# Kernel tuning notes

Hardware: AMD Instinct MI355X
Metric: run time of the kernel (lower is better)

## Reference

```python
import jax, jax.numpy as jnp
import numpy as np

N_NODES = 100000


def _add_self_loops(edge_index, n):
    loops = jnp.arange(n, dtype=edge_index.dtype)
    src = jnp.concatenate([edge_index[0], loops])
    dst = jnp.concatenate([edge_index[1], loops])
    return src, dst


def _gcn_norm(src, dst, n):
    # symmetric normalization with unit edge weights (edge_weight=None)
    w = jnp.ones(src.shape[0], dtype=jnp.float32)
    deg = jax.ops.segment_sum(w, dst, num_segments=n)  # in-degree at dst (col)
    dinv = jnp.where(deg > 0, jax.lax.rsqrt(jnp.maximum(deg, 1.0)), 0.0)
    return dinv[src] * w * dinv[dst]


def _gcn_conv(x, W, b, src, dst, norm, n):
    h = x @ W                              # [N, F_out] linear first (as in PyG GCNConv)
    msg = h[src] * norm[:, None]           # gather + per-edge scale
    agg = jax.ops.segment_sum(msg, dst, num_segments=n)  # scatter-add at dst
    return agg + b


def setup_inputs() -> dict:
    key = jax.random.key(0)
    k1, k2, k3, k4 = jax.random.split(key, 4)
    x = jax.random.normal(k1, (N_NODES, 128), dtype=jnp.float32)
    edge_index = jax.random.randint(k2, (2, 1600000), 0, N_NODES, dtype=jnp.int64)
    W1 = jax.random.normal(k3, (128, 64), dtype=jnp.float32) * 0.08
    b1 = jnp.zeros((64,), dtype=jnp.float32)
    W2 = jax.random.normal(k4, (64, 40), dtype=jnp.float32) * 0.1
    b2 = jnp.zeros((40,), dtype=jnp.float32)
    return {"x": x, "edge_index": edge_index, "W1": W1, "b1": b1, "W2": W2, "b2": b2}


def reference(x, edge_index, W1, b1, W2, b2):
    n = x.shape[0]
    src, dst = _add_self_loops(edge_index, n)
    norm = _gcn_norm(src, dst, n)
    h = _gcn_conv(x, W1, b1, src, dst, norm, n)
    h = jax.nn.relu(h)
    # dropout is identity in eval mode (training=False)
    out = _gcn_conv(h, W2, b2, src, dst, norm, n)
    return out
```

## Files before the change

kernel.cpp:

```cpp
#include <hip/hip_runtime.h>
#include <hip/hip_fp16.h>


#define NPB   128
#define NBCAP 1024


__global__ void k_zero(int* __restrict__ p, int m) {
    int i = blockIdx.x * blockDim.x + threadIdx.x;
    if (i < m) p[i] = 0;
}

__global__ __launch_bounds__(256) void k_hist(const int* __restrict__ dst, int E,
                                              int* __restrict__ bcnt, int nb) {
    __shared__ int h[NBCAP];
    for (int i = threadIdx.x; i < nb; i += 256) h[i] = 0;
    __syncthreads();
    int stride = gridDim.x * 256;
    for (int e = blockIdx.x * 256 + threadIdx.x; e < E; e += stride)
        atomicAdd(&h[dst[e] >> 7], 1);
    __syncthreads();
    for (int i = threadIdx.x; i < nb; i += 256)
        if (h[i]) atomicAdd(&bcnt[i], h[i]);
}

__global__ __launch_bounds__(1024) void k_scan_nb(const int* __restrict__ bcnt,
                                                  int* __restrict__ bbase,
                                                  int* __restrict__ bcur, int nb) {
    __shared__ int tmp[NBCAP];
    int t = threadIdx.x;
    int v = (t < nb) ? bcnt[t] : 0;
    tmp[t] = v;
    __syncthreads();
    for (int ofs = 1; ofs < NBCAP; ofs <<= 1) {
        int u = (t >= ofs) ? tmp[t - ofs] : 0;
        __syncthreads();
        if (t >= ofs) tmp[t] += u;
        __syncthreads();
    }
    if (t < nb) {
        int ex = tmp[t] - v;
        bbase[t] = ex;
        bcur[t] = ex;
        if (t == nb - 1) bbase[nb] = tmp[t];
    }
}

__global__ __launch_bounds__(256) void k_binpass(const int* __restrict__ src,
                                                 const int* __restrict__ dst,
                                                 int* __restrict__ bcur,
                                                 int* __restrict__ pairs,
                                                 int nb, int E) {
    __shared__ int lh[NBCAP];
    __shared__ int lbase[NBCAP];
    for (int i = threadIdx.x; i < nb; i += 256) lh[i] = 0;
    __syncthreads();
    int base = blockIdx.x * 4096;
    int pk[16], bb[16];
#pragma unroll
    for (int k = 0; k < 16; ++k) {
        int e = base + k * 256 + threadIdx.x;
        if (e < E) {
            int d = dst[e];
            int b = d >> 7;
            bb[k] = b;
            pk[k] = src[e] | ((d & (NPB - 1)) << 17);
            atomicAdd(&lh[b], 1);
        } else bb[k] = -1;
    }
    __syncthreads();
    for (int i = threadIdx.x; i < nb; i += 256) {
        int c = lh[i];
        lbase[i] = c ? atomicAdd(&bcur[i], c) : 0;
        lh[i] = 0;
    }
    __syncthreads();
#pragma unroll
    for (int k = 0; k < 16; ++k) {
        if (bb[k] >= 0) {
            int r = atomicAdd(&lh[bb[k]], 1);
            pairs[lbase[bb[k]] + r] = pk[k];
        }
    }
}

__global__ __launch_bounds__(256) void k_bucket_build(const int* __restrict__ pairs,
                                                      const int* __restrict__ bbase,
                                                      int* __restrict__ off,
                                                      int* __restrict__ csrc,
                                                      float* __restrict__ dinv,
                                                      int n, int nb) {
    __shared__ int deg[NPB], sc[NPB], cur[NPB];
    int t = threadIdx.x;
    int bid = blockIdx.x;
    int node0 = bid * NPB;
    int ebeg = bbase[bid], eend = bbase[bid + 1];
    if (t < NPB) deg[t] = 0;
    __syncthreads();
    for (int e = ebeg + t; e < eend; e += 256)
        atomicAdd(&deg[pairs[e] >> 17], 1);
    __syncthreads();
    if (t < NPB) sc[t] = deg[t];
    __syncthreads();
    for (int ofs = 1; ofs < NPB; ofs <<= 1) {
        int u = (t < NPB && t >= ofs) ? sc[t - ofs] : 0;
        __syncthreads();
        if (t < NPB && t >= ofs) sc[t] += u;
        __syncthreads();
    }
    if (t < NPB) {
        int ex = sc[t] - deg[t];
        cur[t] = ex;
        int node = node0 + t;
        if (node < n) {
            off[node] = ebeg + ex;
            dinv[node] = rsqrtf((float)(deg[t] + 1));
        }
    }
    if (t == 0 && bid == nb - 1) off[n] = eend;
    __syncthreads();
    for (int e = ebeg + t; e < eend; e += 256) {
        int pkv = pairs[e];
        int r = atomicAdd(&cur[pkv >> 17], 1);
        csrc[ebeg + r] = pkv & 0x1FFFF;
    }
}


union pk2 { __half2 h[2]; uint2 u; };

__device__ __forceinline__ void h4_acc(const __half* p, float4& a) {
    uint2 u = *(const uint2*)p;
    __half2 h0 = *(__half2*)&u.x, h1 = *(__half2*)&u.y;
    float2 f0 = __half22float2(h0), f1 = __half22float2(h1);
    a.x += f0.x; a.y += f0.y; a.z += f1.x; a.w += f1.y;
}

#define F4ADD(a, b) { (a).x += (b).x; (a).y += (b).y; (a).z += (b).z; (a).w += (b).w; }


__global__ __launch_bounds__(256) void k_gemm1_h(const float* __restrict__ x,
                                                 const float* __restrict__ W,
                                                 __half* __restrict__ h, int n,
                                                 const float* __restrict__ dinv) {
    __shared__ float Ws[128 * 64];
    __shared__ float xsT[128 * 64];
    const int tid = threadIdx.x;
    const int row0 = blockIdx.x * 64;
    {
        const float4* Wg = (const float4*)W;
        float4* Wl = (float4*)Ws;
#pragma unroll
        for (int t = 0; t < 8; ++t) Wl[tid + t * 256] = Wg[tid + t * 256];
    }
    {
        int r = tid & 63, g = tid >> 6;
        int row = row0 + r;
        const float4* xr = (const float4*)(x + (size_t)row * 128);
#pragma unroll
        for (int t = 0; t < 8; ++t) {
            int k0 = g * 32 + t * 4;
            float4 v = (row < n) ? xr[k0 >> 2] : make_float4(0.f, 0.f, 0.f, 0.f);
            xsT[(k0 + 0) * 64 + r] = v.x;
            xsT[(k0 + 1) * 64 + r] = v.y;
            xsT[(k0 + 2) * 64 + r] = v.z;
            xsT[(k0 + 3) * 64 + r] = v.w;
        }
    }
    __syncthreads();

    const int tc = tid & 15;
    const int rg = tid >> 4;
    float acc[4][4];
#pragma unroll
    for (int i = 0; i < 4; ++i)
#pragma unroll
        for (int j = 0; j < 4; ++j) acc[i][j] = 0.f;

#pragma unroll 4
    for (int k = 0; k < 128; ++k) {
        float4 a = *(const float4*)&xsT[k * 64 + rg * 4];
        float4 b = *(const float4*)&Ws[k * 64 + tc * 4];
        acc[0][0] += a.x * b.x; acc[0][1] += a.x * b.y; acc[0][2] += a.x * b.z; acc[0][3] += a.x * b.w;
        acc[1][0] += a.y * b.x; acc[1][1] += a.y * b.y; acc[1][2] += a.y * b.z; acc[1][3] += a.y * b.w;
        acc[2][0] += a.z * b.x; acc[2][1] += a.z * b.y; acc[2][2] += a.z * b.z; acc[2][3] += a.z * b.w;
        acc[3][0] += a.w * b.x; acc[3][1] += a.w * b.y; acc[3][2] += a.w * b.z; acc[3][3] += a.w * b.w;
    }

#pragma unroll
    for (int i = 0; i < 4; ++i) {
        int row = row0 + rg * 4 + i;
        if (row < n) {
            float dd = dinv[row];
            pk2 p;
            p.h[0] = __floats2half2_rn(acc[i][0] * dd, acc[i][1] * dd);
            p.h[1] = __floats2half2_rn(acc[i][2] * dd, acc[i][3] * dd);
            *(uint2*)&h[(size_t)row * 64 + tc * 4] = p.u;
        }
    }
}

__global__ __launch_bounds__(256) void k_gemm2_h(const __half* __restrict__ agg,
                                                 const float* __restrict__ W2,
                                                 __half* __restrict__ h2, int n,
                                                 const float* __restrict__ dinv) {
    __shared__ float Ws[64 * 40];
    __shared__ float hsT[64 * 64];
    const int tid = threadIdx.x;
    const int row0 = blockIdx.x * 64;
    {
        const float4* Wg = (const float4*)W2;
        float4* Wl = (float4*)Ws;
        for (int i = tid; i < 640; i += 256) Wl[i] = Wg[i];
    }
    {
        int r = tid & 63, g = tid >> 6;
        int row = row0 + r;
        const __half* ar = agg + (size_t)row * 64;
#pragma unroll
        for (int t = 0; t < 4; ++t) {
            int k0 = g * 16 + t * 4;
            float4 v = make_float4(0.f, 0.f, 0.f, 0.f);
            if (row < n) {
                uint2 u = *(const uint2*)(ar + k0);
                __half2 h0 = *(__half2*)&u.x, h1 = *(__half2*)&u.y;
                float2 f0 = __half22float2(h0), f1 = __half22float2(h1);
                v = make_float4(f0.x, f0.y, f1.x, f1.y);
            }
            hsT[(k0 + 0) * 64 + r] = v.x > 0.f ? v.x : 0.f;
            hsT[(k0 + 1) * 64 + r] = v.y > 0.f ? v.y : 0.f;
            hsT[(k0 + 2) * 64 + r] = v.z > 0.f ? v.z : 0.f;
            hsT[(k0 + 3) * 64 + r] = v.w > 0.f ? v.w : 0.f;
        }
    }
    __syncthreads();

    const int tc = tid & 15;
    const int rg = tid >> 4;
    if (tc < 10) {
        float acc[4][4];
#pragma unroll
        for (int i = 0; i < 4; ++i)
#pragma unroll
            for (int j = 0; j < 4; ++j) acc[i][j] = 0.f;

#pragma unroll 4
        for (int k = 0; k < 64; ++k) {
            float4 a = *(const float4*)&hsT[k * 64 + rg * 4];
            float4 b = *(const float4*)&Ws[k * 40 + tc * 4];
            acc[0][0] += a.x * b.x; acc[0][1] += a.x * b.y; acc[0][2] += a.x * b.z; acc[0][3] += a.x * b.w;
            acc[1][0] += a.y * b.x; acc[1][1] += a.y * b.y; acc[1][2] += a.y * b.z; acc[1][3] += a.y * b.w;
            acc[2][0] += a.z * b.x; acc[2][1] += a.z * b.y; acc[2][2] += a.z * b.z; acc[2][3] += a.z * b.w;
            acc[3][0] += a.w * b.x; acc[3][1] += a.w * b.y; acc[3][2] += a.w * b.z; acc[3][3] += a.w * b.w;
        }

#pragma unroll
        for (int i = 0; i < 4; ++i) {
            int row = row0 + rg * 4 + i;
            if (row < n) {
                float dd = dinv[row];
                pk2 p;
                p.h[0] = __floats2half2_rn(acc[i][0] * dd, acc[i][1] * dd);
                p.h[1] = __floats2half2_rn(acc[i][2] * dd, acc[i][3] * dd);
                *(uint2*)&h2[(size_t)row * 40 + tc * 4] = p.u;
            }
        }
    }
}


__global__ __launch_bounds__(256) void k_gather1_h(const __half* __restrict__ hs,
                                                   const int* __restrict__ off,
                                                   const int* __restrict__ csrc,
                                                   const float* __restrict__ dinv,
                                                   const float4* __restrict__ b1_4,
                                                   __half* __restrict__ agg, int n) {
    int node = blockIdx.x * 4 + (threadIdx.x >> 6);
    if (node >= n) return;
    int lane = threadIdx.x & 63;
    int g = lane >> 4, q = lane & 15;
    int beg = off[node], end = off[node + 1];
    float4 a0 = make_float4(0.f, 0.f, 0.f, 0.f);
    float4 a1 = make_float4(0.f, 0.f, 0.f, 0.f);
    float4 a2 = make_float4(0.f, 0.f, 0.f, 0.f);
    float4 a3 = make_float4(0.f, 0.f, 0.f, 0.f);
    int j = beg;
    for (; j + 16 <= end; j += 16) {
        int s0 = csrc[j + g], s1 = csrc[j + 4 + g];
        int s2 = csrc[j + 8 + g], s3 = csrc[j + 12 + g];
        h4_acc(hs + (size_t)s0 * 64 + q * 4, a0);
        h4_acc(hs + (size_t)s1 * 64 + q * 4, a1);
        h4_acc(hs + (size_t)s2 * 64 + q * 4, a2);
        h4_acc(hs + (size_t)s3 * 64 + q * 4, a3);
    }
    for (; j + 8 <= end; j += 8) {
        int s0 = csrc[j + g], s1 = csrc[j + 4 + g];
        h4_acc(hs + (size_t)s0 * 64 + q * 4, a0);
        h4_acc(hs + (size_t)s1 * 64 + q * 4, a1);
    }
    for (; j < end; j += 4) {
        int jj = j + g;
        if (jj < end) {
            int s = csrc[jj];
            h4_acc(hs + (size_t)s * 64 + q * 4, a0);
        }
    }
    F4ADD(a0, a1); F4ADD(a2, a3); F4ADD(a0, a2);
    a0.x += __shfl_down(a0.x, 32); a0.y += __shfl_down(a0.y, 32);
    a0.z += __shfl_down(a0.z, 32); a0.w += __shfl_down(a0.w, 32);
    a0.x += __shfl_down(a0.x, 16); a0.y += __shfl_down(a0.y, 16);
    a0.z += __shfl_down(a0.z, 16); a0.w += __shfl_down(a0.w, 16);
    if (lane < 16) {
        float4 s = make_float4(0.f, 0.f, 0.f, 0.f);
        h4_acc(hs + (size_t)node * 64 + q * 4, s);
        float dd = dinv[node];
        float4 b = b1_4[q];
        pk2 p;
        p.h[0] = __floats2half2_rn((a0.x + s.x) * dd + b.x, (a0.y + s.y) * dd + b.y);
        p.h[1] = __floats2half2_rn((a0.z + s.z) * dd + b.z, (a0.w + s.w) * dd + b.w);
        *(uint2*)&agg[(size_t)node * 64 + q * 4] = p.u;
    }
}

__global__ __launch_bounds__(256) void k_gather2_h(const __half* __restrict__ h2s,
                                                   const int* __restrict__ off,
                                                   const int* __restrict__ csrc,
                                                   const float* __restrict__ dinv,
                                                   const float4* __restrict__ b2_4,
                                                   float4* __restrict__ out4, int n) {
    int node = blockIdx.x * 4 + (threadIdx.x >> 6);
    if (node >= n) return;
    int lane = threadIdx.x & 63;
    int g = lane / 10;
    int q = lane - g * 10;
    bool act = g < 6;
    int beg = off[node], end = off[node + 1];
    float4 a0 = make_float4(0.f, 0.f, 0.f, 0.f);
    float4 a1 = make_float4(0.f, 0.f, 0.f, 0.f);
    int j = beg;
    for (; j + 12 <= end; j += 12) {
        if (act) {
            int s0 = csrc[j + g], s1 = csrc[j + 6 + g];
            h4_acc(h2s + (size_t)s0 * 40 + q * 4, a0);
            h4_acc(h2s + (size_t)s1 * 40 + q * 4, a1);
        }
    }
    for (; j < end; j += 6) {
        int jj = j + g;
        if (act && jj < end) {
            int s = csrc[jj];
            h4_acc(h2s + (size_t)s * 40 + q * 4, a0);
        }
    }
    F4ADD(a0, a1);
    float4 r;
    r.x = __shfl_down(a0.x, 30); r.y = __shfl_down(a0.y, 30);
    r.z = __shfl_down(a0.z, 30); r.w = __shfl_down(a0.w, 30);
    if (lane < 30) F4ADD(a0, r);
    r.x = __shfl_down(a0.x, 20); r.y = __shfl_down(a0.y, 20);
    r.z = __shfl_down(a0.z, 20); r.w = __shfl_down(a0.w, 20);
    if (lane < 10) F4ADD(a0, r);
    r.x = __shfl_down(a0.x, 10); r.y = __shfl_down(a0.y, 10);
    r.z = __shfl_down(a0.z, 10); r.w = __shfl_down(a0.w, 10);
    if (lane < 10) F4ADD(a0, r);
    if (lane < 10) {
        float4 s = make_float4(0.f, 0.f, 0.f, 0.f);
        h4_acc(h2s + (size_t)node * 40 + q * 4, s);
        float dd = dinv[node];
        float4 b = b2_4[q];
        float4 o;
        o.x = (a0.x + s.x) * dd + b.x;
        o.y = (a0.y + s.y) * dd + b.y;
        o.z = (a0.z + s.z) * dd + b.z;
        o.w = (a0.w + s.w) * dd + b.w;
        out4[node * 10 + q] = o;
    }
}


__global__ void k_init_deg(float* __restrict__ deg, int n) {
    int i = blockIdx.x * blockDim.x + threadIdx.x;
    if (i < n) deg[i] = 1.0f;
}

__global__ void k_deg(const int* __restrict__ dst, int E, float* __restrict__ deg) {
    int i = blockIdx.x * blockDim.x + threadIdx.x;
    if (i < E) atomicAdd(&deg[dst[i]], 1.0f);
}

__global__ void k_rsqrt(float* __restrict__ deg, int n) {
    int i = blockIdx.x * blockDim.x + threadIdx.x;
    if (i < n) deg[i] = rsqrtf(deg[i]);
}

__global__ __launch_bounds__(256) void k_gemm1_f(const float* __restrict__ x,
                                                 const float* __restrict__ W,
                                                 float* __restrict__ h, int n) {
    __shared__ float Ws[128 * 64];
    __shared__ float xsT[128 * 64];
    const int tid = threadIdx.x;
    const int row0 = blockIdx.x * 64;
    {
        const float4* Wg = (const float4*)W;
        float4* Wl = (float4*)Ws;
#pragma unroll
        for (int t = 0; t < 8; ++t) Wl[tid + t * 256] = Wg[tid + t * 256];
    }
    {
        int r = tid & 63, g = tid >> 6;
        int row = row0 + r;
        const float4* xr = (const float4*)(x + (size_t)row * 128);
#pragma unroll
        for (int t = 0; t < 8; ++t) {
            int k0 = g * 32 + t * 4;
            float4 v = (row < n) ? xr[k0 >> 2] : make_float4(0.f, 0.f, 0.f, 0.f);
            xsT[(k0 + 0) * 64 + r] = v.x;
            xsT[(k0 + 1) * 64 + r] = v.y;
            xsT[(k0 + 2) * 64 + r] = v.z;
            xsT[(k0 + 3) * 64 + r] = v.w;
        }
    }
    __syncthreads();
    const int tc = tid & 15;
    const int rg = tid >> 4;
    float acc[4][4];
#pragma unroll
    for (int i = 0; i < 4; ++i)
#pragma unroll
        for (int j = 0; j < 4; ++j) acc[i][j] = 0.f;
#pragma unroll 4
    for (int k = 0; k < 128; ++k) {
        float4 a = *(const float4*)&xsT[k * 64 + rg * 4];
        float4 b = *(const float4*)&Ws[k * 64 + tc * 4];
        acc[0][0] += a.x * b.x; acc[0][1] += a.x * b.y; acc[0][2] += a.x * b.z; acc[0][3] += a.x * b.w;
        acc[1][0] += a.y * b.x; acc[1][1] += a.y * b.y; acc[1][2] += a.y * b.z; acc[1][3] += a.y * b.w;
        acc[2][0] += a.z * b.x; acc[2][1] += a.z * b.y; acc[2][2] += a.z * b.z; acc[2][3] += a.z * b.w;
        acc[3][0] += a.w * b.x; acc[3][1] += a.w * b.y; acc[3][2] += a.w * b.z; acc[3][3] += a.w * b.w;
    }
#pragma unroll
    for (int i = 0; i < 4; ++i) {
        int row = row0 + rg * 4 + i;
        if (row < n)
            *(float4*)&h[(size_t)row * 64 + tc * 4] =
                make_float4(acc[i][0], acc[i][1], acc[i][2], acc[i][3]);
    }
}

__global__ __launch_bounds__(256) void k_gemm2_f(const float* __restrict__ agg,
                                                 const float* __restrict__ W2,
                                                 float* __restrict__ h2, int n) {
    __shared__ float Ws[64 * 40];
    __shared__ float hsT[64 * 64];
    const int tid = threadIdx.x;
    const int row0 = blockIdx.x * 64;
    {
        const float4* Wg = (const float4*)W2;
        float4* Wl = (float4*)Ws;
        for (int i = tid; i < 640; i += 256) Wl[i] = Wg[i];
    }
    {
        int r = tid & 63, g = tid >> 6;
        int row = row0 + r;
        const float4* ar = (const float4*)(agg + (size_t)row * 64);
#pragma unroll
        for (int t = 0; t < 4; ++t) {
            int k0 = g * 16 + t * 4;
            float4 v = (row < n) ? ar[k0 >> 2] : make_float4(0.f, 0.f, 0.f, 0.f);
            hsT[(k0 + 0) * 64 + r] = v.x > 0.f ? v.x : 0.f;
            hsT[(k0 + 1) * 64 + r] = v.y > 0.f ? v.y : 0.f;
            hsT[(k0 + 2) * 64 + r] = v.z > 0.f ? v.z : 0.f;
            hsT[(k0 + 3) * 64 + r] = v.w > 0.f ? v.w : 0.f;
        }
    }
    __syncthreads();
    const int tc = tid & 15;
    const int rg = tid >> 4;
    if (tc < 10) {
        float acc[4][4];
#pragma unroll
        for (int i = 0; i < 4; ++i)
#pragma unroll
            for (int j = 0; j < 4; ++j) acc[i][j] = 0.f;
#pragma unroll 4
        for (int k = 0; k < 64; ++k) {
            float4 a = *(const float4*)&hsT[k * 64 + rg * 4];
            float4 b = *(const float4*)&Ws[k * 40 + tc * 4];
            acc[0][0] += a.x * b.x; acc[0][1] += a.x * b.y; acc[0][2] += a.x * b.z; acc[0][3] += a.x * b.w;
            acc[1][0] += a.y * b.x; acc[1][1] += a.y * b.y; acc[1][2] += a.y * b.z; acc[1][3] += a.y * b.w;
            acc[2][0] += a.z * b.x; acc[2][1] += a.z * b.y; acc[2][2] += a.z * b.z; acc[2][3] += a.z * b.w;
            acc[3][0] += a.w * b.x; acc[3][1] += a.w * b.y; acc[3][2] += a.w * b.z; acc[3][3] += a.w * b.w;
        }
#pragma unroll
        for (int i = 0; i < 4; ++i) {
            int row = row0 + rg * 4 + i;
            if (row < n)
                *(float4*)&h2[(size_t)row * 40 + tc * 4] =
                    make_float4(acc[i][0], acc[i][1], acc[i][2], acc[i][3]);
        }
    }
}

__global__ void k_init_agg1(const float* __restrict__ h, const float* __restrict__ dinv,
                            const float* __restrict__ b1, float* __restrict__ agg, int n) {
    int idx = blockIdx.x * blockDim.x + threadIdx.x;
    if (idx < n * 64) {
        int i = idx >> 6, f = idx & 63;
        float d = dinv[i];
        agg[idx] = h[idx] * d * d + b1[f];
    }
}

__global__ __launch_bounds__(256) void k_scatter1(const float* __restrict__ h,
                                                  const int* __restrict__ src,
                                                  const int* __restrict__ dst,
                                                  const float* __restrict__ dinv,
                                                  float* __restrict__ agg, int E) {
    int e = blockIdx.x * 4 + (threadIdx.x >> 6);
    if (e >= E) return;
    int f = threadIdx.x & 63;
    int s = src[e], d = dst[e];
    float w = dinv[s] * dinv[d];
    atomicAdd(&agg[d * 64 + f], h[s * 64 + f] * w);
}

__global__ void k_init_out(const float* __restrict__ h2, const float* __restrict__ dinv,
                           const float* __restrict__ b2, float* __restrict__ out, int n) {
    int idx = blockIdx.x * blockDim.x + threadIdx.x;
    if (idx < n * 40) {
        int i = idx / 40;
        int f = idx - i * 40;
        float d = dinv[i];
        out[idx] = h2[idx] * d * d + b2[f];
    }
}

__global__ __launch_bounds__(256) void k_scatter2(const float* __restrict__ h2,
                                                  const int* __restrict__ src,
                                                  const int* __restrict__ dst,
                                                  const float* __restrict__ dinv,
                                                  float* __restrict__ out, int E) {
    int idx = blockIdx.x * blockDim.x + threadIdx.x;
    int total = E * 40;
    if (idx >= total) return;
    int e = idx / 40;
    int f = idx - e * 40;
    int s = src[e], d = dst[e];
    float w = dinv[s] * dinv[d];
    atomicAdd(&out[d * 40 + f], h2[s * 40 + f] * w);
}

extern "C" void kernel_launch(void* const* d_in, const int* in_sizes, int n_in,
                              void* d_out, int out_size, void* d_ws, size_t ws_size,
                              hipStream_t stream) {
    const float* x  = (const float*)d_in[0];
    const int*   ei = (const int*)d_in[1];
    const float* W1 = (const float*)d_in[2];
    const float* b1 = (const float*)d_in[3];
    const float* W2 = (const float*)d_in[4];
    const float* b2 = (const float*)d_in[5];
    float* out = (float*)d_out;

    const int n = in_sizes[0] / 128;
    const int E = in_sizes[1] / 2;
    const int* src = ei;
    const int* dst = ei + E;

    char* ws = (char*)d_ws;
    const size_t MB = 1 << 20;
    float*  dinv   = (float*)(ws);
    int*    off    = (int*)  (ws + 512 * 1024);
    int*    bcnt   = (int*)  (ws + 1 * MB);
    int*    bbase  = (int*)  (ws + 1 * MB + 8 * 1024);
    int*    bcur   = (int*)  (ws + 1 * MB + 16 * 1024);
    __half* hs_h   = (__half*)(ws + 2 * MB);
    __half* agg1_h = (__half*)(ws + 15 * MB);
    __half* h2s_h  = hs_h;
    int*    pairs  = (int*)  (ws + 28 * MB);
    int*    csrc   = (int*)  (ws + 35 * MB);
    size_t needed_fast = 35 * MB + (size_t)E * 4;

    const int nb = (n + NPB - 1) / NPB;

    if (ws_size >= needed_fast && nb <= NBCAP && n <= (1 << 17)) {
        k_zero<<<(nb + 255) / 256, 256, 0, stream>>>(bcnt, nb);
        k_hist<<<512, 256, 0, stream>>>(dst, E, bcnt, nb);
        k_scan_nb<<<1, 1024, 0, stream>>>(bcnt, bbase, bcur, nb);
        k_binpass<<<(E + 4095) / 4096, 256, 0, stream>>>(src, dst, bcur, pairs, nb, E);
        k_bucket_build<<<nb, 256, 0, stream>>>(pairs, bbase, off, csrc, dinv, n, nb);

        k_gemm1_h<<<(n + 63) / 64, 256, 0, stream>>>(x, W1, hs_h, n, dinv);
        k_gather1_h<<<(n + 3) / 4, 256, 0, stream>>>(hs_h, off, csrc, dinv,
                                                     (const float4*)b1, agg1_h, n);
        k_gemm2_h<<<(n + 63) / 64, 256, 0, stream>>>(agg1_h, W2, h2s_h, n, dinv);
        k_gather2_h<<<(n + 3) / 4, 256, 0, stream>>>(h2s_h, off, csrc, dinv,
                                                     (const float4*)b2, (float4*)out, n);
    } else {
        float* hlin = (float*)(ws + 2 * MB);
        float* agg1 = (float*)(ws + 28 * MB);
        k_init_deg<<<(n + 255) / 256, 256, 0, stream>>>(dinv, n);
        k_deg<<<(E + 255) / 256, 256, 0, stream>>>(dst, E, dinv);
        k_rsqrt<<<(n + 255) / 256, 256, 0, stream>>>(dinv, n);
        k_gemm1_f<<<(n + 63) / 64, 256, 0, stream>>>(x, W1, hlin, n);
        k_init_agg1<<<(n * 64 + 255) / 256, 256, 0, stream>>>(hlin, dinv, b1, agg1, n);
        k_scatter1<<<(E + 3) / 4, 256, 0, stream>>>(hlin, src, dst, dinv, agg1, E);
        k_gemm2_f<<<(n + 63) / 64, 256, 0, stream>>>(agg1, W2, hlin, n);
        k_init_out<<<(n * 40 + 255) / 256, 256, 0, stream>>>(hlin, dinv, b2, out, n);
        int total2 = E * 40;
        k_scatter2<<<(total2 + 255) / 256, 256, 0, stream>>>(hlin, src, dst, dinv, out, E);
    }
}
```

Measured before the change: 208.4 us.

## Widen gather loads to 16B per lane and use persistent grid-stride waves

Both CSR gather kernels now read 8 halves (uint4) per lane instead of 4. This lets each wavefront process more edges at once: 8 rows per step instead of 4 in layer 1, and 12 instead of 6 in layer 2. The kernels also switch from one block per 4 nodes to a fixed grid of 2048 blocks whose waves stride over nodes, which cuts launch and tail overhead. The trade-off is fewer independent accumulators in layer 2 and a longer shuffle reduction. Alignment holds because the 40-half rows are 80 bytes, a multiple of 16.

```diff
diff --git a/kernel.cpp b/kernel.cpp
--- a/kernel.cpp
+++ b/kernel.cpp
@@ -128,15 +128,27 @@
 
 
 union pk2 { __half2 h[2]; uint2 u; };
-
-__device__ __forceinline__ void h4_acc(const __half* p, float4& a) {
-    uint2 u = *(const uint2*)p;
+union pk4 { __half2 h[4]; uint4 u; };
+
+#define F4ADD(a, b) { (a).x += (b).x; (a).y += (b).y; (a).z += (b).z; (a).w += (b).w; }
+
+__device__ __forceinline__ void acc8f(float4& lo, float4& hi, uint4 u) {
     __half2 h0 = *(__half2*)&u.x, h1 = *(__half2*)&u.y;
+    __half2 h2v = *(__half2*)&u.z, h3v = *(__half2*)&u.w;
     float2 f0 = __half22float2(h0), f1 = __half22float2(h1);
-    a.x += f0.x; a.y += f0.y; a.z += f1.x; a.w += f1.y;
-}
-
-#define F4ADD(a, b) { (a).x += (b).x; (a).y += (b).y; (a).z += (b).z; (a).w += (b).w; }
+    float2 f2 = __half22float2(h2v), f3 = __half22float2(h3v);
+    lo.x += f0.x; lo.y += f0.y; lo.z += f1.x; lo.w += f1.y;
+    hi.x += f2.x; hi.y += f2.y; hi.z += f3.x; hi.w += f3.y;
+}
+
+__device__ __forceinline__ void redstep(float4& lo, float4& hi, int delta, bool act) {
+    float4 rl, rh;
+    rl.x = __shfl_down(lo.x, delta); rl.y = __shfl_down(lo.y, delta);
+    rl.z = __shfl_down(lo.z, delta); rl.w = __shfl_down(lo.w, delta);
+    rh.x = __shfl_down(hi.x, delta); rh.y = __shfl_down(hi.y, delta);
+    rh.z = __shfl_down(hi.z, delta); rh.w = __shfl_down(hi.w, delta);
+    if (act) { F4ADD(lo, rl); F4ADD(hi, rh); }
+}
 
 
 __global__ __launch_bounds__(256) void k_gemm1_h(const float* __restrict__ x,
@@ -273,52 +285,60 @@
                                                    const int* __restrict__ off,
                                                    const int* __restrict__ csrc,
                                                    const float* __restrict__ dinv,
-                                                   const float4* __restrict__ b1_4,
-                                                   __half* __restrict__ agg, int n) {
-    int node = blockIdx.x * 4 + (threadIdx.x >> 6);
-    if (node >= n) return;
+                                                   const float* __restrict__ bias1,
+                                                   __half* __restrict__ agg1,
+                                                   int n, int nwaves) {
+    int wid = (blockIdx.x * 256 + threadIdx.x) >> 6;
     int lane = threadIdx.x & 63;
-    int g = lane >> 4, q = lane & 15;
-    int beg = off[node], end = off[node + 1];
-    float4 a0 = make_float4(0.f, 0.f, 0.f, 0.f);
-    float4 a1 = make_float4(0.f, 0.f, 0.f, 0.f);
-    float4 a2 = make_float4(0.f, 0.f, 0.f, 0.f);
-    float4 a3 = make_float4(0.f, 0.f, 0.f, 0.f);
-    int j = beg;
-    for (; j + 16 <= end; j += 16) {
-        int s0 = csrc[j + g], s1 = csrc[j + 4 + g];
-        int s2 = csrc[j + 8 + g], s3 = csrc[j + 12 + g];
-        h4_acc(hs + (size_t)s0 * 64 + q * 4, a0);
-        h4_acc(hs + (size_t)s1 * 64 + q * 4, a1);
-        h4_acc(hs + (size_t)s2 * 64 + q * 4, a2);
-        h4_acc(hs + (size_t)s3 * 64 + q * 4, a3);
-    }
-    for (; j + 8 <= end; j += 8) {
-        int s0 = csrc[j + g], s1 = csrc[j + 4 + g];
-        h4_acc(hs + (size_t)s0 * 64 + q * 4, a0);
-        h4_acc(hs + (size_t)s1 * 64 + q * 4, a1);
-    }
-    for (; j < end; j += 4) {
-        int jj = j + g;
-        if (jj < end) {
-            int s = csrc[jj];
-            h4_acc(hs + (size_t)s * 64 + q * 4, a0);
-        }
-    }
-    F4ADD(a0, a1); F4ADD(a2, a3); F4ADD(a0, a2);
-    a0.x += __shfl_down(a0.x, 32); a0.y += __shfl_down(a0.y, 32);
-    a0.z += __shfl_down(a0.z, 32); a0.w += __shfl_down(a0.w, 32);
-    a0.x += __shfl_down(a0.x, 16); a0.y += __shfl_down(a0.y, 16);
-    a0.z += __shfl_down(a0.z, 16); a0.w += __shfl_down(a0.w, 16);
-    if (lane < 16) {
-        float4 s = make_float4(0.f, 0.f, 0.f, 0.f);
-        h4_acc(hs + (size_t)node * 64 + q * 4, s);
-        float dd = dinv[node];
-        float4 b = b1_4[q];
-        pk2 p;
-        p.h[0] = __floats2half2_rn((a0.x + s.x) * dd + b.x, (a0.y + s.y) * dd + b.y);
-        p.h[1] = __floats2half2_rn((a0.z + s.z) * dd + b.z, (a0.w + s.w) * dd + b.w);
-        *(uint2*)&agg[(size_t)node * 64 + q * 4] = p.u;
+    int g = lane >> 3, q = lane & 7;
+    for (int node = wid; node < n; node += nwaves) {
+        int beg = off[node], end = off[node + 1];
+        float4 a0 = make_float4(0.f, 0.f, 0.f, 0.f);
+        float4 a1 = make_float4(0.f, 0.f, 0.f, 0.f);
+        float4 c0 = make_float4(0.f, 0.f, 0.f, 0.f);
+        float4 c1 = make_float4(0.f, 0.f, 0.f, 0.f);
+        int j = beg;
+        for (; j + 16 <= end; j += 16) {
+            int s0 = csrc[j + g];
+            int s1 = csrc[j + 8 + g];
+            uint4 u0 = *(const uint4*)(hs + ((size_t)s0 << 6) + (q << 3));
+            uint4 u1 = *(const uint4*)(hs + ((size_t)s1 << 6) + (q << 3));
+            acc8f(a0, a1, u0);
+            acc8f(c0, c1, u1);
+        }
+        for (; j + 8 <= end; j += 8) {
+            int s0 = csrc[j + g];
+            uint4 u0 = *(const uint4*)(hs + ((size_t)s0 << 6) + (q << 3));
+            acc8f(a0, a1, u0);
+        }
+        if (j + g < end) {
+            int s0 = csrc[j + g];
+            uint4 u0 = *(const uint4*)(hs + ((size_t)s0 << 6) + (q << 3));
+            acc8f(a0, a1, u0);
+        }
+        F4ADD(a0, c0); F4ADD(a1, c1);
+        redstep(a0, a1, 32, lane < 32);
+        redstep(a0, a1, 16, lane < 16);
+        redstep(a0, a1, 8,  lane < 8);
+        if (lane < 8) {
+            float dd = dinv[node];
+            uint4 us = *(const uint4*)(hs + ((size_t)node << 6) + (q << 3));
+            float4 slo = make_float4(0.f, 0.f, 0.f, 0.f);
+            float4 shi = make_float4(0.f, 0.f, 0.f, 0.f);
+            acc8f(slo, shi, us);
+            float4 blo = *(const float4*)(bias1 + q * 8);
+            float4 bhi = *(const float4*)(bias1 + q * 8 + 4);
+            pk4 p;
+            p.h[0] = __floats2half2_rn((a0.x + slo.x) * dd + blo.x,
+                                       (a0.y + slo.y) * dd + blo.y);
+            p.h[1] = __floats2half2_rn((a0.z + slo.z) * dd + blo.z,
+                                       (a0.w + slo.w) * dd + blo.w);
+            p.h[2] = __floats2half2_rn((a1.x + shi.x) * dd + bhi.x,
+                                       (a1.y + shi.y) * dd + bhi.y);
+            p.h[3] = __floats2half2_rn((a1.z + shi.z) * dd + bhi.z,
+                                       (a1.w + shi.w) * dd + bhi.w);
+            *(uint4*)&agg1[((size_t)node << 6) + (q << 3)] = p.u;
+        }
     }
 }
 
@@ -326,54 +346,55 @@
                                                    const int* __restrict__ off,
                                                    const int* __restrict__ csrc,
                                                    const float* __restrict__ dinv,
-                                                   const float4* __restrict__ b2_4,
-                                                   float4* __restrict__ out4, int n) {
-    int node = blockIdx.x * 4 + (threadIdx.x >> 6);
-    if (node >= n) return;
+                                                   const float* __restrict__ b2,
+                                                   float* __restrict__ out,
+                                                   int n, int nwaves) {
+    int wid = (blockIdx.x * 256 + threadIdx.x) >> 6;
     int lane = threadIdx.x & 63;
-    int g = lane / 10;
-    int q = lane - g * 10;
-    bool act = g < 6;
-    int beg = off[node], end = off[node + 1];
-    float4 a0 = make_float4(0.f, 0.f, 0.f, 0.f);
-    float4 a1 = make_float4(0.f, 0.f, 0.f, 0.f);
-    int j = beg;
-    for (; j + 12 <= end; j += 12) {
-        if (act) {
-            int s0 = csrc[j + g], s1 = csrc[j + 6 + g];
-            h4_acc(h2s + (size_t)s0 * 40 + q * 4, a0);
-            h4_acc(h2s + (size_t)s1 * 40 + q * 4, a1);
-        }
-    }
-    for (; j < end; j += 6) {
-        int jj = j + g;
-        if (act && jj < end) {
-            int s = csrc[jj];
-            h4_acc(h2s + (size_t)s * 40 + q * 4, a0);
-        }
-    }
-    F4ADD(a0, a1);
-    float4 r;
-    r.x = __shfl_down(a0.x, 30); r.y = __shfl_down(a0.y, 30);
-    r.z = __shfl_down(a0.z, 30); r.w = __shfl_down(a0.w, 30);
-    if (lane < 30) F4ADD(a0, r);
-    r.x = __shfl_down(a0.x, 20); r.y = __shfl_down(a0.y, 20);
-    r.z = __shfl_down(a0.z, 20); r.w = __shfl_down(a0.w, 20);
-    if (lane < 10) F4ADD(a0, r);
-    r.x = __shfl_down(a0.x, 10); r.y = __shfl_down(a0.y, 10);
-    r.z = __shfl_down(a0.z, 10); r.w = __shfl_down(a0.w, 10);
-    if (lane < 10) F4ADD(a0, r);
-    if (lane < 10) {
-        float4 s = make_float4(0.f, 0.f, 0.f, 0.f);
-        h4_acc(h2s + (size_t)node * 40 + q * 4, s);
-        float dd = dinv[node];
-        float4 b = b2_4[q];
-        float4 o;
-        o.x = (a0.x + s.x) * dd + b.x;
-        o.y = (a0.y + s.y) * dd + b.y;
-        o.z = (a0.z + s.z) * dd + b.z;
-        o.w = (a0.w + s.w) * dd + b.w;
-        out4[node * 10 + q] = o;
+    int g = lane / 5;
+    int q = lane - g * 5;
+    bool act = lane < 60;
+    for (int node = wid; node < n; node += nwaves) {
+        int beg = off[node], end = off[node + 1];
+        float4 a0 = make_float4(0.f, 0.f, 0.f, 0.f);
+        float4 a1 = make_float4(0.f, 0.f, 0.f, 0.f);
+        int j = beg;
+        for (; j + 12 <= end; j += 12) {
+            if (act) {
+                int s0 = csrc[j + g];
+                uint4 u0 = *(const uint4*)(h2s + (size_t)s0 * 40 + q * 8);
+                acc8f(a0, a1, u0);
+            }
+        }
+        if (act && j + g < end) {
+            int s0 = csrc[j + g];
+            uint4 u0 = *(const uint4*)(h2s + (size_t)s0 * 40 + q * 8);
+            acc8f(a0, a1, u0);
+        }
+        redstep(a0, a1, 30, lane < 30);
+        redstep(a0, a1, 15, lane < 15);
+        redstep(a0, a1, 10, lane < 5);
+        redstep(a0, a1, 5,  lane < 5);
+        if (lane < 5) {
+            float dd = dinv[node];
+            uint4 us = *(const uint4*)(h2s + (size_t)node * 40 + lane * 8);
+            float4 slo = make_float4(0.f, 0.f, 0.f, 0.f);
+            float4 shi = make_float4(0.f, 0.f, 0.f, 0.f);
+            acc8f(slo, shi, us);
+            float4 blo = *(const float4*)(b2 + lane * 8);
+            float4 bhi = *(const float4*)(b2 + lane * 8 + 4);
+            float4 o0, o1;
+            o0.x = (a0.x + slo.x) * dd + blo.x;
+            o0.y = (a0.y + slo.y) * dd + blo.y;
+            o0.z = (a0.z + slo.z) * dd + blo.z;
+            o0.w = (a0.w + slo.w) * dd + blo.w;
+            o1.x = (a1.x + shi.x) * dd + bhi.x;
+            o1.y = (a1.y + shi.y) * dd + bhi.y;
+            o1.z = (a1.z + shi.z) * dd + bhi.z;
+            o1.w = (a1.w + shi.w) * dd + bhi.w;
+            *(float4*)&out[(size_t)node * 40 + lane * 8] = o0;
+            *(float4*)&out[(size_t)node * 40 + lane * 8 + 4] = o1;
+        }
     }
 }
 
@@ -588,12 +609,13 @@
         k_binpass<<<(E + 4095) / 4096, 256, 0, stream>>>(src, dst, bcur, pairs, nb, E);
         k_bucket_build<<<nb, 256, 0, stream>>>(pairs, bbase, off, csrc, dinv, n, nb);
 
+        const int GB = 2048;
+        const int NW = GB * 4;
         k_gemm1_h<<<(n + 63) / 64, 256, 0, stream>>>(x, W1, hs_h, n, dinv);
-        k_gather1_h<<<(n + 3) / 4, 256, 0, stream>>>(hs_h, off, csrc, dinv,
-                                                     (const float4*)b1, agg1_h, n);
+        k_gather1_h<<<GB, 256, 0, stream>>>(hs_h, off, csrc, dinv, b1, agg1_h, n, NW);
+
         k_gemm2_h<<<(n + 63) / 64, 256, 0, stream>>>(agg1_h, W2, h2s_h, n, dinv);
-        k_gather2_h<<<(n + 3) / 4, 256, 0, stream>>>(h2s_h, off, csrc, dinv,
-                                                     (const float4*)b2, (float4*)out, n);
+        k_gather2_h<<<GB, 256, 0, stream>>>(h2s_h, off, csrc, dinv, b2, out, n, NW);
     } else {
         float* hlin = (float*)(ws + 2 * MB);
         float* agg1 = (float*)(ws + 28 * MB);
```

New measurement: 199.2 us. 4.4% less time.
